# Optimization experiments

Hardware: AMD Instinct MI355X
Metric: run time of the kernel (lower is better)

## Reference

```python
import jax, jax.numpy as jnp
import numpy as np

B, T, C = 2, 2048, 1024
N_HEAD, N_KV_HEAD, N_GLOBAL_HEAD = 16, 8, 8
HEAD_DIM = C // N_HEAD  # 64
Q_PER_KV = N_HEAD // N_KV_HEAD  # 2
N_GLOBAL_KV = N_GLOBAL_HEAD // Q_PER_KV  # 4
VE_GATE_CH = 32


def setup_inputs() -> dict:
    key = jax.random.key(0)
    ks = jax.random.split(key, 8)
    x = jax.random.normal(ks[0], (B, T, C), jnp.float32)
    ve = jax.random.normal(ks[1], (B, T, N_KV_HEAD * HEAD_DIM), jnp.float32)
    # rotary cos/sin: [T, 1, head_dim//2]
    half = HEAD_DIM // 2
    inv_freq = 1.0 / (10000.0 ** (np.arange(half, dtype=np.float32) / half))
    ang = np.arange(T, dtype=np.float32)[:, None] * inv_freq[None, :]
    cos = jnp.asarray(np.cos(ang))[:, None, :]
    sin = jnp.asarray(np.sin(ang))[:, None, :]
    s = 0.02
    Wq = jax.random.normal(ks[2], (C, N_HEAD * HEAD_DIM), jnp.float32) * s
    Wk = jax.random.normal(ks[3], (C, N_KV_HEAD * HEAD_DIM), jnp.float32) * s
    Wv = jax.random.normal(ks[4], (C, N_KV_HEAD * HEAD_DIM), jnp.float32) * s
    Wproj = jax.random.normal(ks[5], (C, C), jnp.float32) * s
    Wgate = jax.random.normal(ks[6], (VE_GATE_CH, N_KV_HEAD), jnp.float32) * s
    return {"x": x, "ve": ve, "cos": cos, "sin": sin, "Wq": Wq, "Wk": Wk,
            "Wv": Wv, "Wproj": Wproj, "Wgate": Wgate, "window": 512}


def _rope(x, cos, sin):
    # x: [B,T,H,D]; cos/sin: [T,1,D/2]
    d = x.shape[-1] // 2
    x1, x2 = x[..., :d], x[..., d:]
    return jnp.concatenate([x1 * cos + x2 * sin, -x1 * sin + x2 * cos], axis=-1)


def _rmsnorm(x):
    eps = jnp.finfo(x.dtype).eps
    return x * jax.lax.rsqrt(jnp.mean(x * x, axis=-1, keepdims=True) + eps)


def _attn(q, k, v, mask):
    # q,k,v: [B,T,H,D]; mask: [T,T] bool (True = allowed)
    scale = 1.0 / jnp.sqrt(jnp.asarray(q.shape[-1], q.dtype))
    scores = jnp.einsum('bqhd,bkhd->bhqk', q, k) * scale
    scores = jnp.where(mask[None, None], scores, jnp.finfo(scores.dtype).min)
    p = jax.nn.softmax(scores, axis=-1)
    return jnp.einsum('bhqk,bkhd->bqhd', p, v)


def reference(x, ve, cos, sin, Wq, Wk, Wv, Wproj, Wgate, window):
    q = (x @ Wq).reshape(B, T, N_HEAD, HEAD_DIM)
    k = (x @ Wk).reshape(B, T, N_KV_HEAD, HEAD_DIM)
    v = (x @ Wv).reshape(B, T, N_KV_HEAD, HEAD_DIM)
    # value-embedding gate
    gate = 2.0 * jax.nn.sigmoid(x[..., :VE_GATE_CH] @ Wgate)  # [B,T,n_kv]
    v = v + gate[..., None] * ve.reshape(B, T, N_KV_HEAD, HEAD_DIM)
    q, k = _rope(q, cos, sin), _rope(k, cos, sin)
    q, k = _rmsnorm(q), _rmsnorm(k)
    # split global / local heads
    qg, ql = q[:, :, :N_GLOBAL_HEAD], q[:, :, N_GLOBAL_HEAD:]
    kg, kl = k[:, :, :N_GLOBAL_KV], k[:, :, N_GLOBAL_KV:]
    vg, vl = v[:, :, :N_GLOBAL_KV], v[:, :, N_GLOBAL_KV:]
    # GQA: expand kv heads
    kg, vg = jnp.repeat(kg, Q_PER_KV, axis=2), jnp.repeat(vg, Q_PER_KV, axis=2)
    kl, vl = jnp.repeat(kl, Q_PER_KV, axis=2), jnp.repeat(vl, Q_PER_KV, axis=2)
    i = jnp.arange(T)[:, None]
    j = jnp.arange(T)[None, :]
    causal = j <= i
    local_mask = causal & (j >= i - window)  # flash window_size=(window, 0)
    yg = _attn(qg, kg, vg, causal)
    yl = _attn(ql, kl, vl, local_mask)
    y = jnp.concatenate([yg, yl], axis=2).reshape(B, T, C)
    return y @ Wproj
```

## Files before the change

kernel.cpp:

```cpp
#include <hip/hip_runtime.h>
#include <hip/hip_bf16.h>

#define BB 2
#define TT 2048
#define CC 1024
#define NH 16
#define NKV 8
#define HD 64

typedef __attribute__((ext_vector_type(8))) short short8;
typedef __attribute__((ext_vector_type(4))) float float4v;

__device__ __forceinline__ ushort f2bf(float f) {
    __hip_bfloat16 h = __float2bfloat16(f);
    union { __hip_bfloat16 h; ushort u; } v; v.h = h; return v.u;
}

__device__ __forceinline__ void gload16(const ushort* g, ushort* l) {
    __builtin_amdgcn_global_load_lds(
        (const __attribute__((address_space(1))) unsigned int*)g,
        (__attribute__((address_space(3))) unsigned int*)l, 16, 0, 0);
}

__device__ __forceinline__ void transpose_tile(
    const float* __restrict__ src, ushort* __restrict__ dst,
    int Kd, int Nd, int kt, int nt, float* tile )
{
    const int tid = threadIdx.x;
    {
        int r = tid >> 2, c = (tid & 3) * 16;
        #pragma unroll
        for (int i = 0; i < 4; i++) {
            float4 v = *(const float4*)&src[(size_t)(kt + r) * Nd + nt + c + i * 4];
            tile[r * 65 + c + i * 4 + 0] = v.x;
            tile[r * 65 + c + i * 4 + 1] = v.y;
            tile[r * 65 + c + i * 4 + 2] = v.z;
            tile[r * 65 + c + i * 4 + 3] = v.w;
        }
    }
    __syncthreads();
    {
        int n = tid >> 2, k = (tid & 3) * 16;
        #pragma unroll
        for (int i = 0; i < 2; i++) {
            ushort u[8];
            #pragma unroll
            for (int j = 0; j < 8; j++) u[j] = f2bf(tile[(k + i * 8 + j) * 65 + n]);
            *(uint4*)&dst[(size_t)(nt + n) * Kd + kt + k + i * 8] = *(uint4*)u;
        }
    }
}

__global__ __launch_bounds__(256) void prep_kernel(
    const float* __restrict__ x, ushort* __restrict__ xb,
    const float* __restrict__ Wq, const float* __restrict__ Wk,
    const float* __restrict__ Wv, const float* __restrict__ Wproj,
    ushort* __restrict__ WqkvT, ushort* __restrict__ WpT)
{
    __shared__ float tile[64 * 65];
    const int bid = blockIdx.x;
    if (bid < 4096) {
        int i = (bid * 256 + threadIdx.x) * 4;
        float4 v = *(const float4*)&x[i];
        xb[i + 0] = f2bf(v.x);
        xb[i + 1] = f2bf(v.y);
        xb[i + 2] = f2bf(v.z);
        xb[i + 3] = f2bf(v.w);
        return;
    }
    int t = bid - 4096;
    if (t < 256) {
        transpose_tile(Wq, WqkvT, 1024, 1024, (t >> 4) * 64, (t & 15) * 64, tile);
    } else if (t < 384) {
        t -= 256;
        transpose_tile(Wk, WqkvT + (size_t)1024 * 1024, 1024, 512, (t >> 3) * 64, (t & 7) * 64, tile);
    } else if (t < 512) {
        t -= 384;
        transpose_tile(Wv, WqkvT + (size_t)1536 * 1024, 1024, 512, (t >> 3) * 64, (t & 7) * 64, tile);
    } else {
        t -= 512;
        transpose_tile(Wproj, WpT, 1024, 1024, (t >> 4) * 64, (t & 15) * 64, tile);
    }
}

template<int BM>
__global__ __launch_bounds__(256) void gemm_bt_kernel(
    const ushort* __restrict__ A, const ushort* __restrict__ Bt,
    float* __restrict__ Cp, int M, int N, int K, int ldc)
{
    constexpr int RT = BM / 32;
    __shared__ ushort As[BM][32];
    __shared__ ushort Bs[128][32];

    const int m0 = blockIdx.x * BM;
    const int n0 = blockIdx.y * 128;
    const int tid = threadIdx.x;
    const int lane = tid & 63;
    const int w = tid >> 6;
    const int lr = lane & 15, lc = lane >> 4;
    const int wm = (w >> 1) * (BM / 2), wn = (w & 1) * 64;

    float4v acc[RT][4] = {};

    for (int k0 = 0; k0 < K; k0 += 32) {
        #pragma unroll
        for (int s = 0; s < BM / 64; s++) {
            int rb = w * (BM / 4) + s * 16;
            gload16(&A[(size_t)(m0 + rb + (lane >> 2)) * K + k0 + (lane & 3) * 8], &As[rb][0]);
        }
        #pragma unroll
        for (int s = 0; s < 2; s++) {
            int rb = w * 32 + s * 16;
            gload16(&Bt[(size_t)(n0 + rb + (lane >> 2)) * K + k0 + (lane & 3) * 8], &Bs[rb][0]);
        }
        __syncthreads();

        short8 af[RT], bf[4];
        #pragma unroll
        for (int t = 0; t < RT; t++)
            af[t] = *(const short8*)&As[wm + t * 16 + lr][lc * 8];
        #pragma unroll
        for (int t = 0; t < 4; t++)
            bf[t] = *(const short8*)&Bs[wn + t * 16 + lr][lc * 8];
        #pragma unroll
        for (int rt = 0; rt < RT; rt++)
            #pragma unroll
            for (int ct = 0; ct < 4; ct++)
                acc[rt][ct] = __builtin_amdgcn_mfma_f32_16x16x32_bf16(af[rt], bf[ct], acc[rt][ct], 0, 0, 0);
        __syncthreads();
    }

    #pragma unroll
    for (int rt = 0; rt < RT; rt++)
        #pragma unroll
        for (int ct = 0; ct < 4; ct++)
            #pragma unroll
            for (int r = 0; r < 4; r++) {
                int row = m0 + wm + rt * 16 + lc * 4 + r;
                int col = n0 + wn + ct * 16 + lr;
                Cp[(size_t)row * ldc + col] = acc[rt][ct][r];
            }
}

__global__ __launch_bounds__(256) void qkv_post_kernel(
    const float* __restrict__ qkv, const float* __restrict__ x,
    const float* __restrict__ ve, const float* __restrict__ cosb,
    const float* __restrict__ sinb, const float* __restrict__ wgate,
    ushort* __restrict__ Qb, ushort* __restrict__ Kb, ushort* __restrict__ Vn)
{
    const int bt = blockIdx.x;
    const int b = bt >> 11, t = bt & 2047;
    const int tid = threadIdx.x;
    const int lane = tid & 63;
    const int w = tid >> 6;
    __shared__ float gateS[8];

    {
        int g = tid >> 5, i = tid & 31;
        float p = x[(size_t)bt * CC + i] * wgate[i * 8 + g];
        #pragma unroll
        for (int off = 16; off; off >>= 1) p += __shfl_down(p, off, 32);
        if (i == 0) gateS[g] = 2.f / (1.f + __expf(-p));
    }
    __syncthreads();

    const float c = cosb[t * 32 + (lane & 31)];
    const float s = sinb[t * 32 + (lane & 31)];
    for (int hh = w; hh < 24; hh += 4) {
        const float* z = &qkv[(size_t)bt * 2048 + hh * 64];
        float v = z[lane];
        float other = __shfl_xor(v, 32);
        float x1 = (lane < 32) ? v : other;
        float x2 = (lane < 32) ? other : v;
        float val = (lane < 32) ? (x1 * c + x2 * s) : (-x1 * s + x2 * c);
        float ss = val * val;
        #pragma unroll
        for (int off = 32; off; off >>= 1) ss += __shfl_xor(ss, off);
        float scale = rsqrtf(ss * (1.f / 64.f) + 1.1920929e-07f);
        ushort ob = f2bf(val * scale);
        if (hh < 16) Qb[(((size_t)b * NH + hh) * TT + t) * HD + lane] = ob;
        else         Kb[(((size_t)b * NKV + (hh - 16)) * TT + t) * HD + lane] = ob;
    }

    for (int e = tid; e < NKV * HD; e += 256) {
        int kh = e >> 6, d = e & 63;
        float v = qkv[(size_t)bt * 2048 + 1536 + e] + gateS[kh] * ve[(size_t)bt * 512 + e];
        Vn[(((size_t)b * NKV + kh) * TT + t) * HD + d] = f2bf(v);
    }
}

__global__ __launch_bounds__(256) void v_transpose_kernel(
    const ushort* __restrict__ Vn, ushort* __restrict__ Vt)
{
    __shared__ ushort tile[64][72];
    const int t0 = blockIdx.x * 64;
    const int bh = blockIdx.y;
    const ushort* src = &Vn[(size_t)bh * TT * HD + (size_t)t0 * HD];
    ushort* dst = &Vt[(size_t)bh * HD * TT + t0];
    const int tid = threadIdx.x;
    {
        int r = tid >> 2, c = (tid & 3) * 16;
        #pragma unroll
        for (int i = 0; i < 2; i++)
            *(uint4*)&tile[r][c + i * 8] = *(const uint4*)&src[(size_t)r * HD + c + i * 8];
    }
    __syncthreads();
    {
        int d = tid >> 2, c = (tid & 3) * 16;
        #pragma unroll
        for (int i = 0; i < 2; i++) {
            ushort u[8];
            #pragma unroll
            for (int j = 0; j < 8; j++) u[j] = tile[c + i * 8 + j][d];
            *(uint4*)&dst[(size_t)d * TT + c + i * 8] = *(uint4*)u;
        }
    }
}

__global__ __launch_bounds__(256) void attn_kernel(
    const ushort* __restrict__ Qb, const ushort* __restrict__ Kb,
    const ushort* __restrict__ Vt, ushort* __restrict__ Yb,
    const int* __restrict__ winp)
{
    const int gid = blockIdx.x;
    int b, h, qw;
    if (gid < 1024) { qw = 63 - (gid >> 4); h = (gid >> 1) & 7; b = gid & 1; }
    else { int j = gid - 1024; qw = 63 - (j >> 4); h = 8 + ((j >> 1) & 7); b = j & 1; }

    const int q0 = qw * 32;
    const int kvh = h >> 1;
    const bool local = (h >= 8);
    int window = *winp;
    if (window < 0 || window > TT) window = TT;
    const int tid = threadIdx.x;
    const int w = tid >> 6;
    const int lane = tid & 63;
    const int lr = lane & 15, lc = lane >> 4;

    __shared__ ushort Ps[4][16][72];
    __shared__ float4v Ol[4][4][64];
    __shared__ float Ll[4][16];

    const ushort* qbase = &Qb[(((size_t)b * NH + h) * TT + q0) * HD];
    short8 qf[2][2];
    #pragma unroll
    for (int rt = 0; rt < 2; rt++)
        #pragma unroll
        for (int xh = 0; xh < 2; xh++)
            qf[rt][xh] = *(const short8*)&qbase[(size_t)(rt * 16 + lr) * HD + xh * 32 + lc * 8];

    float4v o[2][4] = {};
    float l_[2] = {0.f, 0.f};

    const ushort* Kbase = &Kb[((size_t)b * NKV + kvh) * TT * HD];
    const ushort* Vbase = &Vt[((size_t)b * NKV + kvh) * HD * TT];

    const int qlast = q0 + 31;
    int jstart = 0;
    if (local) { int js = q0 - window; if (js > 0) jstart = js & ~63; }
    const int j0first = jstart + w * 64;

    short8 kf[4][2];
    if (j0first <= qlast) {
        #pragma unroll
        for (int jt = 0; jt < 4; jt++) {
            const ushort* kp = &Kbase[(size_t)(j0first + jt * 16 + lr) * HD + lc * 8];
            kf[jt][0] = *(const short8*)kp;
            kf[jt][1] = *(const short8*)(kp + 32);
        }
    }

    for (int j0 = j0first; j0 <= qlast; j0 += 256) {
        short8 vf[4][2];
        #pragma unroll
        for (int ct = 0; ct < 4; ct++) {
            const ushort* vp = &Vbase[(size_t)(ct * 16 + lr) * TT + j0 + lc * 8];
            vf[ct][0] = *(const short8*)vp;
            vf[ct][1] = *(const short8*)(vp + 32);
        }
        short8 kn[4][2];
        const bool more = (j0 + 256 <= qlast);
        if (more) {
            #pragma unroll
            for (int jt = 0; jt < 4; jt++) {
                const ushort* kp = &Kbase[(size_t)(j0 + 256 + jt * 16 + lr) * HD + lc * 8];
                kn[jt][0] = *(const short8*)kp;
                kn[jt][1] = *(const short8*)(kp + 32);
            }
        }

        float4v st[2][4];
        #pragma unroll
        for (int jt = 0; jt < 4; jt++)
            #pragma unroll
            for (int rt = 0; rt < 2; rt++) {
                float4v z = {};
                z = __builtin_amdgcn_mfma_f32_16x16x32_bf16(kf[jt][0], qf[rt][0], z, 0, 0, 0);
                z = __builtin_amdgcn_mfma_f32_16x16x32_bf16(kf[jt][1], qf[rt][1], z, 0, 0, 0);
                st[rt][jt] = z;
            }

        const bool need_c = (j0 + 63 > q0);
        const bool need_w = local && (j0 < qlast - window);

        #pragma unroll
        for (int rt = 0; rt < 2; rt++) {
            const int qrow = q0 + rt * 16 + lr;
            float p[4][4];
            if (need_c || need_w) {
                #pragma unroll
                for (int jt = 0; jt < 4; jt++)
                    #pragma unroll
                    for (int r = 0; r < 4; r++) {
                        int key = j0 + jt * 16 + lc * 4 + r;
                        bool ok = (key <= qrow) && (!local || key >= qrow - window);
                        p[jt][r] = ok ? __expf(st[rt][jt][r] * 0.125f) : 0.f;
                    }
            } else {
                #pragma unroll
                for (int jt = 0; jt < 4; jt++)
                    #pragma unroll
                    for (int r = 0; r < 4; r++)
                        p[jt][r] = __expf(st[rt][jt][r] * 0.125f);
            }
            float s0 = (p[0][0] + p[0][1]) + (p[0][2] + p[0][3]);
            float s1 = (p[1][0] + p[1][1]) + (p[1][2] + p[1][3]);
            float s2 = (p[2][0] + p[2][1]) + (p[2][2] + p[2][3]);
            float s3 = (p[3][0] + p[3][1]) + (p[3][2] + p[3][3]);
            l_[rt] += (s0 + s1) + (s2 + s3);

            #pragma unroll
            for (int jt = 0; jt < 4; jt++) {
                ushort4 u;
                u.x = f2bf(p[jt][0]); u.y = f2bf(p[jt][1]);
                u.z = f2bf(p[jt][2]); u.w = f2bf(p[jt][3]);
                *(ushort4*)&Ps[w][lr][jt * 16 + lc * 4] = u;
            }
            short8 pb0 = *(const short8*)&Ps[w][lr][lc * 8];
            short8 pb1 = *(const short8*)&Ps[w][lr][32 + lc * 8];
            #pragma unroll
            for (int ct = 0; ct < 4; ct++) {
                o[rt][ct] = __builtin_amdgcn_mfma_f32_16x16x32_bf16(vf[ct][0], pb0, o[rt][ct], 0, 0, 0);
                o[rt][ct] = __builtin_amdgcn_mfma_f32_16x16x32_bf16(vf[ct][1], pb1, o[rt][ct], 0, 0, 0);
            }
        }

        if (more) {
            #pragma unroll
            for (int jt = 0; jt < 4; jt++) {
                kf[jt][0] = kn[jt][0];
                kf[jt][1] = kn[jt][1];
            }
        }
    }

    #pragma unroll
    for (int rt = 0; rt < 2; rt++) {
        l_[rt] += __shfl_xor(l_[rt], 16);
        l_[rt] += __shfl_xor(l_[rt], 32);
    }

    #pragma unroll
    for (int rt = 0; rt < 2; rt++) {
        #pragma unroll
        for (int ct = 0; ct < 4; ct++) Ol[w][ct][lane] = o[rt][ct];
        if (lc == 0) Ll[w][lr] = l_[rt];
        __syncthreads();

        {
            const int ct = w;
            float ltot = (Ll[0][lr] + Ll[1][lr]) + (Ll[2][lr] + Ll[3][lr]);
            float inv = 1.f / fmaxf(ltot, 1e-20f);
            float4v a0 = Ol[0][ct][lane], a1 = Ol[1][ct][lane];
            float4v a2 = Ol[2][ct][lane], a3 = Ol[3][ct][lane];
            int qrow = q0 + rt * 16 + lr;
            ushort4 u;
            u.x = f2bf(((a0[0] + a1[0]) + (a2[0] + a3[0])) * inv);
            u.y = f2bf(((a0[1] + a1[1]) + (a2[1] + a3[1])) * inv);
            u.z = f2bf(((a0[2] + a1[2]) + (a2[2] + a3[2])) * inv);
            u.w = f2bf(((a0[3] + a1[3]) + (a2[3] + a3[3])) * inv);
            *(ushort4*)&Yb[((size_t)b * TT + qrow) * CC + h * 64 + ct * 16 + lc * 4] = u;
        }
        if (rt == 0) __syncthreads();
    }
}

extern "C" void kernel_launch(void* const* d_in, const int* in_sizes, int n_in,
                              void* d_out, int out_size, void* d_ws, size_t ws_size,
                              hipStream_t stream) {
    (void)in_sizes; (void)n_in; (void)out_size; (void)ws_size;
    const float* x     = (const float*)d_in[0];
    const float* ve    = (const float*)d_in[1];
    const float* cosb  = (const float*)d_in[2];
    const float* sinb  = (const float*)d_in[3];
    const float* Wq    = (const float*)d_in[4];
    const float* Wk    = (const float*)d_in[5];
    const float* Wv    = (const float*)d_in[6];
    const float* Wproj = (const float*)d_in[7];
    const float* Wgate = (const float*)d_in[8];
    const int*   winp  = (const int*)d_in[9];
    float* out = (float*)d_out;

    char* ws = (char*)d_ws;
    float*  qkv   = (float*)ws;
    ushort* Yb    = (ushort*)ws;
    ushort* xb    = (ushort*)(ws + 33554432);
    ushort* Vnb   = (ushort*)(ws + 33554432);
    ushort* WqkvT = (ushort*)(ws + 41943040);
    ushort* WpT   = (ushort*)(ws + 46137344);
    ushort* Qb    = (ushort*)(ws + 48234496);
    ushort* Kb    = (ushort*)(ws + 56623104);
    ushort* Vtb   = (ushort*)(ws + 60817408);

    dim3 blk(256);
    prep_kernel<<<dim3(4864), blk, 0, stream>>>(x, xb, Wq, Wk, Wv, Wproj, WqkvT, WpT);
    gemm_bt_kernel<128><<<dim3(32, 16), blk, 0, stream>>>(xb, WqkvT, qkv, 4096, 2048, 1024, 2048);
    qkv_post_kernel<<<dim3(BB * TT), blk, 0, stream>>>(qkv, x, ve, cosb, sinb, Wgate, Qb, Kb, Vnb);
    v_transpose_kernel<<<dim3(TT / 64, BB * NKV), blk, 0, stream>>>(Vnb, Vtb);
    attn_kernel<<<dim3(2048), blk, 0, stream>>>(Qb, Kb, Vtb, Yb, winp);
    gemm_bt_kernel<64><<<dim3(64, 8), blk, 0, stream>>>(Yb, WpT, out, 4096, 1024, 1024, 1024);
}
```

Measured before the change: 222.2 us.

## Use 8 waves per attention block and remap blocks to XCDs by KV head

The attention kernel now runs with 512 threads (8 waves) per block, each wave handling a 64-key slice with a 512-key stride, so every query tile splits its keys across twice as many waves. Block indices are remapped so that blocks sharing a batch/KV-head pair land on the same XCD, which should improve L2 reuse of K/V. The cross-wave reduction grows to 8 partials, with half the waves finalizing each row tile. The cost is more LDS per block, likely fewer resident blocks, and more reduction and sync work for short causal or windowed ranges.

```diff
diff --git a/kernel.cpp b/kernel.cpp
--- a/kernel.cpp
+++ b/kernel.cpp
@@ -217,18 +217,23 @@
     }
 }
 
-__global__ __launch_bounds__(256) void attn_kernel(
+__global__ __launch_bounds__(512) void attn_kernel(
     const ushort* __restrict__ Qb, const ushort* __restrict__ Kb,
     const ushort* __restrict__ Vt, ushort* __restrict__ Yb,
     const int* __restrict__ winp)
 {
     const int gid = blockIdx.x;
-    int b, h, qw;
-    if (gid < 1024) { qw = 63 - (gid >> 4); h = (gid >> 1) & 7; b = gid & 1; }
-    else { int j = gid - 1024; qw = 63 - (j >> 4); h = 8 + ((j >> 1) & 7); b = j & 1; }
+    const int xcd = gid & 7;
+    const int slot = gid >> 3;
+    const int csel = slot >> 7;
+    const int rest = slot & 127;
+    const int combo = xcd + csel * 8;
+    const int b = combo >> 3;
+    const int kvh = combo & 7;
+    const int h = kvh * 2 + (rest >> 6);
+    const int qw = 63 - (rest & 63);
 
     const int q0 = qw * 32;
-    const int kvh = h >> 1;
     const bool local = (h >= 8);
     int window = *winp;
     if (window < 0 || window > TT) window = TT;
@@ -237,9 +242,9 @@
     const int lane = tid & 63;
     const int lr = lane & 15, lc = lane >> 4;
 
-    __shared__ ushort Ps[4][16][72];
-    __shared__ float4v Ol[4][4][64];
-    __shared__ float Ll[4][16];
+    __shared__ ushort Ps[8][16][72];
+    __shared__ float4v Ol[8][4][64];
+    __shared__ float Ll[8][16];
 
     const ushort* qbase = &Qb[(((size_t)b * NH + h) * TT + q0) * HD];
     short8 qf[2][2];
@@ -270,7 +275,7 @@
         }
     }
 
-    for (int j0 = j0first; j0 <= qlast; j0 += 256) {
+    for (int j0 = j0first; j0 <= qlast; j0 += 512) {
         short8 vf[4][2];
         #pragma unroll
         for (int ct = 0; ct < 4; ct++) {
@@ -279,11 +284,11 @@
             vf[ct][1] = *(const short8*)(vp + 32);
         }
         short8 kn[4][2];
-        const bool more = (j0 + 256 <= qlast);
+        const bool more = (j0 + 512 <= qlast);
         if (more) {
             #pragma unroll
             for (int jt = 0; jt < 4; jt++) {
-                const ushort* kp = &Kbase[(size_t)(j0 + 256 + jt * 16 + lr) * HD + lc * 8];
+                const ushort* kp = &Kbase[(size_t)(j0 + 512 + jt * 16 + lr) * HD + lc * 8];
                 kn[jt][0] = *(const short8*)kp;
                 kn[jt][1] = *(const short8*)(kp + 32);
             }
@@ -367,18 +372,25 @@
         if (lc == 0) Ll[w][lr] = l_[rt];
         __syncthreads();
 
-        {
-            const int ct = w;
-            float ltot = (Ll[0][lr] + Ll[1][lr]) + (Ll[2][lr] + Ll[3][lr]);
+        const bool mine = (rt == 0) ? (w < 4) : (w >= 4);
+        if (mine) {
+            const int ct = w & 3;
+            float ltot = 0.f;
+            #pragma unroll
+            for (int ww = 0; ww < 8; ww++) ltot += Ll[ww][lr];
             float inv = 1.f / fmaxf(ltot, 1e-20f);
-            float4v a0 = Ol[0][ct][lane], a1 = Ol[1][ct][lane];
-            float4v a2 = Ol[2][ct][lane], a3 = Ol[3][ct][lane];
+            float4v acc = Ol[0][ct][lane];
+            #pragma unroll
+            for (int ww = 1; ww < 8; ww++) {
+                float4v a = Ol[ww][ct][lane];
+                acc[0] += a[0]; acc[1] += a[1]; acc[2] += a[2]; acc[3] += a[3];
+            }
             int qrow = q0 + rt * 16 + lr;
             ushort4 u;
-            u.x = f2bf(((a0[0] + a1[0]) + (a2[0] + a3[0])) * inv);
-            u.y = f2bf(((a0[1] + a1[1]) + (a2[1] + a3[1])) * inv);
-            u.z = f2bf(((a0[2] + a1[2]) + (a2[2] + a3[2])) * inv);
-            u.w = f2bf(((a0[3] + a1[3]) + (a2[3] + a3[3])) * inv);
+            u.x = f2bf(acc[0] * inv);
+            u.y = f2bf(acc[1] * inv);
+            u.z = f2bf(acc[2] * inv);
+            u.w = f2bf(acc[3] * inv);
             *(ushort4*)&Yb[((size_t)b * TT + qrow) * CC + h * 64 + ct * 16 + lc * 4] = u;
         }
         if (rt == 0) __syncthreads();
@@ -417,6 +429,6 @@
     gemm_bt_kernel<128><<<dim3(32, 16), blk, 0, stream>>>(xb, WqkvT, qkv, 4096, 2048, 1024, 2048);
     qkv_post_kernel<<<dim3(BB * TT), blk, 0, stream>>>(qkv, x, ve, cosb, sinb, Wgate, Qb, Kb, Vnb);
     v_transpose_kernel<<<dim3(TT / 64, BB * NKV), blk, 0, stream>>>(Vnb, Vtb);
-    attn_kernel<<<dim3(2048), blk, 0, stream>>>(Qb, Kb, Vtb, Yb, winp);
+    attn_kernel<<<dim3(2048), dim3(512), 0, stream>>>(Qb, Kb, Vtb, Yb, winp);
     gemm_bt_kernel<64><<<dim3(64, 8), blk, 0, stream>>>(Yb, WpT, out, 4096, 1024, 1024, 1024);
 }
```

Result: slower. 250.8 us (+12.9%).
